# Performance work log

Hardware: AMD Instinct MI355X
Metric: run time of the kernel (lower is better)

## Reference

```python
import jax, jax.numpy as jnp
import numpy as np


def setup_inputs() -> dict:
    key = jax.random.key(0)
    ks = jax.random.split(key, 4)
    B, S, H = 1, 2048, 2048
    E, I = 32, 768
    scale_h = 1.0 / np.sqrt(H)
    scale_i = 1.0 / np.sqrt(I)
    return {
        "hidden_states": jax.random.normal(ks[0], (B, S, H), dtype=jnp.float32),
        "gate_w": jax.random.normal(ks[1], (E, H), dtype=jnp.float32) * scale_h,
        "gate_up_proj": jax.random.normal(ks[2], (E, H, 2 * I), dtype=jnp.float32) * scale_h,
        "down_proj": jax.random.normal(ks[3], (E, I, H), dtype=jnp.float32) * scale_i,
    }


TOP_K = 4


def reference(hidden_states, gate_w, gate_up_proj, down_proj):
    B, S, H = hidden_states.shape
    x = hidden_states.reshape(-1, H)                      # [T, H]
    T = x.shape[0]

    # Router: softmax -> top-k -> renormalize -> scatter back to dense [T, E]
    router_logits = x @ gate_w.T                          # [T, E]
    probs = jax.nn.softmax(router_logits.astype(jnp.float32), axis=-1)
    top_w, top_idx = jax.lax.top_k(probs, TOP_K)          # [T, K]
    top_w = top_w / jnp.sum(top_w, axis=-1, keepdims=True)
    top_w = top_w.astype(x.dtype)
    router_weights = jnp.zeros_like(router_logits).at[
        jnp.arange(T)[:, None], top_idx
    ].set(top_w)                                          # [T, E]

    # Experts (eval path): every expert processes every token, then weight & sum.
    gate_up = jnp.einsum("th,ehi->eti", x, gate_up_proj)  # [E, T, 2I]
    gate, up = jnp.split(gate_up, 2, axis=-1)
    h = up * jax.nn.silu(gate)                            # [E, T, I]
    expert_out = jnp.einsum("eti,eih->eth", h, down_proj)  # [E, T, H]
    out = jnp.einsum("eth,te->th", expert_out, router_weights)  # [T, H]

    return out.reshape(B, S, H), router_logits
```

## Files before the change

### kernel.cpp

```cpp
#include <hip/hip_runtime.h>
#include <hip/hip_bf16.h>

#define T_TOK 2048
#define H_DIM 2048
#define E_NUM 32
#define I_DIM 768
#define TOPK  4
#define S4    (T_TOK * TOPK)

typedef __attribute__((ext_vector_type(8))) short bf16x8;
typedef __attribute__((ext_vector_type(4))) float f32x4;

__device__ __forceinline__ unsigned pk2(float a, float b) {
    __hip_bfloat16 ha = __float2bfloat16(a);
    __hip_bfloat16 hb = __float2bfloat16(b);
    unsigned short ua = *(unsigned short*)&ha;
    unsigned short ub = *(unsigned short*)&hb;
    return (unsigned)ua | ((unsigned)ub << 16);
}

#define MFMA16(a, b, c) __builtin_amdgcn_mfma_f32_16x16x32_bf16(a, b, c, 0, 0, 0)

__global__ __launch_bounds__(256) void zero_kernel(uint4* __restrict__ p, int n16)
{
    int i = blockIdx.x * 256 + threadIdx.x;
    if (i < n16) p[i] = (uint4){0u, 0u, 0u, 0u};
}

__global__ __launch_bounds__(64) void router_kernel(
    const float* __restrict__ x, const float* __restrict__ gate_w,
    float* __restrict__ logits_out, int* __restrict__ cnt,
    int* __restrict__ tok_list, float* __restrict__ tok_w)
{
    const int t = blockIdx.x;
    const int lane = threadIdx.x;
    __shared__ float xs[H_DIM];
    const float4* __restrict__ xv = (const float4*)(x + (size_t)t * H_DIM);
    float4* xsv = (float4*)xs;
#pragma unroll
    for (int i = 0; i < H_DIM / 4 / 64; ++i) xsv[lane + i * 64] = xv[lane + i * 64];
    __syncthreads();

    const int e = lane & 31;
    const int half = lane >> 5;
    const float4* __restrict__ wv = (const float4*)(gate_w + (size_t)e * H_DIM) + half * (H_DIM / 8);
    const float4* __restrict__ xh = ((const float4*)xs) + half * (H_DIM / 8);
    float acc = 0.f;
#pragma unroll 4
    for (int i = 0; i < H_DIM / 8; ++i) {
        float4 w4 = wv[i], x4 = xh[i];
        acc += w4.x * x4.x + w4.y * x4.y + w4.z * x4.z + w4.w * x4.w;
    }
    acc += __shfl_xor(acc, 32, 64);
    if (lane < 32) logits_out[(size_t)t * E_NUM + e] = acc;

    float v = acc;
    float topv[TOPK]; int topi[TOPK];
#pragma unroll
    for (int r = 0; r < TOPK; ++r) {
        float bv = v; int bi = e;
#pragma unroll
        for (int off = 16; off >= 1; off >>= 1) {
            float ov = __shfl_xor(bv, off, 32);
            int   oi = __shfl_xor(bi, off, 32);
            if (ov > bv || (ov == bv && oi < bi)) { bv = ov; bi = oi; }
        }
        topv[r] = bv; topi[r] = bi;
        if (e == bi) v = -1e30f;
    }
    if (lane == 0) {
        float w[TOPK]; float s = 0.f;
#pragma unroll
        for (int r = 0; r < TOPK; ++r) { w[r] = expf(topv[r] - topv[0]); s += w[r]; }
        float inv = 1.f / s;
#pragma unroll
        for (int r = 0; r < TOPK; ++r) {
            int pos = atomicAdd(&cnt[topi[r]], 1);
            tok_list[topi[r] * T_TOK + pos] = t;
            tok_w  [topi[r] * T_TOK + pos] = w[r] * inv;
        }
    }
}

__global__ void scan_kernel(const int* __restrict__ cnt, int* __restrict__ slot_base)
{
    if (threadIdx.x == 0) {
        int s = 0;
        for (int e = 0; e < E_NUM; ++e) { slot_base[e] = s; s += cnt[e]; }
        slot_base[E_NUM] = s;
    }
}

__global__ __launch_bounds__(256) void gather_kernel(
    const float* __restrict__ x, const int* __restrict__ cnt,
    const int* __restrict__ slot_base, const int* __restrict__ tok_list,
    unsigned short* __restrict__ xg_t)
{
    const int e = blockIdx.x;
    const int count = cnt[e];
    const int m0 = blockIdx.y * 8;
    if (m0 >= count) return;
    const int s8   = threadIdx.x >> 5;
    const int kc31 = threadIdx.x & 31;
    const int m = m0 + s8;
    if (m >= count) return;
    const int tok  = tok_list[e * T_TOK + m];
    const int slot = slot_base[e] + m;
    const float* __restrict__ src = x + (size_t)tok * H_DIM;
#pragma unroll
    for (int kcq = 0; kcq < 8; ++kcq) {
        const int kc = kcq * 32 + kc31;
        float4 a = *(const float4*)(src + kc * 8);
        float4 b = *(const float4*)(src + kc * 8 + 4);
        uint4 o;
        o.x = pk2(a.x, a.y); o.y = pk2(a.z, a.w);
        o.z = pk2(b.x, b.y); o.w = pk2(b.z, b.w);
        *(uint4*)(xg_t + ((size_t)kc * S4 + slot) * 8) = o;
    }
}

#define GU_NC (H_DIM / 128)
__global__ __launch_bounds__(512, 4) void gateup_mfma(
    const unsigned short* __restrict__ xg_t, const float* __restrict__ gup_w,
    const int* __restrict__ cnt, const int* __restrict__ slot_base,
    const float* __restrict__ tok_w, unsigned short* __restrict__ h_t)
{
    const int e  = blockIdx.x;
    const int nt = blockIdx.y;
    const int mt = blockIdx.z;
    const int count = cnt[e];
    if (mt * 256 >= count) return;
    const int tid  = threadIdx.x;
    const int lane = tid & 63;
    const int w    = tid >> 6;
    const int base = slot_base[e];
    const int l16  = lane & 15, lg = lane >> 4;

    __shared__ unsigned short Bls[2][2][16 * 32 * 8];
    __shared__ float wls[256];

    if (tid < 256) {
        int m = mt * 256 + tid; if (m >= count) m = count - 1;
        wls[tid] = tok_w[e * T_TOK + m];
    }

    int m0 = mt * 256 + w * 32 + l16;      if (m0 >= count) m0 = count - 1;
    int m1 = mt * 256 + w * 32 + 16 + l16; if (m1 >= count) m1 = count - 1;
    const unsigned short* a0b = xg_t + (size_t)(base + m0) * 8;
    const unsigned short* a1b = xg_t + (size_t)(base + m1) * 8;

    const int bhalf = tid >> 8;
    const int sub   = (tid >> 7) & 1;
    const int t7    = tid & 127;
    const int kb    = (t7 >> 3) * 2;
    const int n4    = (t7 & 7) * 4;
    const int k8    = kb & 7;
    const int kbh   = kb >> 3;
    const float* __restrict__ bbase =
        gup_w + ((size_t)e * H_DIM + kb) * (2 * I_DIM) + (size_t)bhalf * I_DIM + nt * 32 + n4;

    float4 sv0[2], sv1[2];

#define GU_LOAD(C) do { _Pragma("unroll") for (int q2 = 0; q2 < 2; ++q2) { \
        const int q = sub + q2 * 2; \
        const float* s_ = bbase + (size_t)((C) * 128 + q * 32) * (2 * I_DIM); \
        sv0[q2] = *(const float4*)s_; \
        sv1[q2] = *(const float4*)(s_ + 2 * I_DIM); } } while (0)
#define GU_WRITE(BUF) do { _Pragma("unroll") for (int q2 = 0; q2 < 2; ++q2) { \
        const int q = sub + q2 * 2; \
        unsigned short* bw_ = &Bls[BUF][bhalf][((q * 4 + kbh) * 32) * 8]; \
        float p0[4] = {sv0[q2].x, sv0[q2].y, sv0[q2].z, sv0[q2].w}; \
        float p1[4] = {sv1[q2].x, sv1[q2].y, sv1[q2].z, sv1[q2].w}; \
        _Pragma("unroll") for (int j = 0; j < 4; ++j) \
            *(unsigned*)&bw_[(n4 + j) * 8 + k8] = pk2(p0[j], p1[j]); } } while (0)

    f32x4 accg[2][2], accu[2][2];
#pragma unroll
    for (int i = 0; i < 2; ++i)
#pragma unroll
        for (int f = 0; f < 2; ++f) { accg[i][f] = {0.f,0.f,0.f,0.f}; accu[i][f] = {0.f,0.f,0.f,0.f}; }

    GU_LOAD(0);
    GU_WRITE(0);

    for (int c = 0; c < GU_NC; ++c) {
        const int buf = c & 1;
        __syncthreads();
        if (c + 1 < GU_NC) GU_LOAD(c + 1);
#pragma unroll
        for (int s = 0; s < 4; ++s) {
            const size_t aoff = (size_t)(c * 16 + s * 4 + lg) * (S4 * 8);
            bf16x8 a0 = *(const bf16x8*)(a0b + aoff);
            bf16x8 a1 = *(const bf16x8*)(a1b + aoff);
            const unsigned short* bg_ = &Bls[buf][0][((s * 4 + lg) * 32 + l16) * 8];
            const unsigned short* bu_ = &Bls[buf][1][((s * 4 + lg) * 32 + l16) * 8];
            bf16x8 g0 = *(const bf16x8*)(bg_);
            bf16x8 g1 = *(const bf16x8*)(bg_ + 128);
            bf16x8 u0 = *(const bf16x8*)(bu_);
            bf16x8 u1 = *(const bf16x8*)(bu_ + 128);
            accg[0][0] = MFMA16(a0, g0, accg[0][0]);
            accg[0][1] = MFMA16(a0, g1, accg[0][1]);
            accu[0][0] = MFMA16(a0, u0, accu[0][0]);
            accu[0][1] = MFMA16(a0, u1, accu[0][1]);
            accg[1][0] = MFMA16(a1, g0, accg[1][0]);
            accg[1][1] = MFMA16(a1, g1, accg[1][1]);
            accu[1][0] = MFMA16(a1, u0, accu[1][0]);
            accu[1][1] = MFMA16(a1, u1, accu[1][1]);
        }
        if (c + 1 < GU_NC) GU_WRITE((c + 1) & 1);
    }
#undef GU_LOAD
#undef GU_WRITE

#pragma unroll
    for (int i = 0; i < 2; ++i) {
        const int mloc = w * 32 + i * 16 + lg * 4;
#pragma unroll
        for (int r = 0; r < 4; ++r) {
            const int mrow = mt * 256 + mloc + r;
            if (mrow < count) {
                const float wgt = wls[mloc + r];
                const size_t slot = (size_t)(base + mrow);
#pragma unroll
                for (int f = 0; f < 2; ++f) {
                    const int col = nt * 32 + f * 16 + l16;
                    float g = accg[i][f][r], u = accu[i][f][r];
                    float sv = g / (1.f + expf(-g));
                    __hip_bfloat16 hb = __float2bfloat16(wgt * u * sv);
                    h_t[((size_t)(col >> 3) * S4 + slot) * 8 + (col & 7)] = *(unsigned short*)&hb;
                }
            }
        }
    }
}

#define DN_NC (I_DIM / 128)
__global__ __launch_bounds__(512, 4) void down_mfma(
    const unsigned short* __restrict__ h_t, const float* __restrict__ down_w,
    const int* __restrict__ cnt, const int* __restrict__ slot_base,
    const int* __restrict__ tok_list, float* __restrict__ out)
{
    const int e  = blockIdx.x;
    const int nt = blockIdx.y;
    const int mt = blockIdx.z;
    const int count = cnt[e];
    if (mt * 256 >= count) return;
    const int tid  = threadIdx.x;
    const int lane = tid & 63;
    const int w    = tid >> 6;
    const int base = slot_base[e];
    const int l16  = lane & 15, lg = lane >> 4;

    __shared__ unsigned short Bls[2][16 * 64 * 8];
    __shared__ int toks[256];

    if (tid < 256) {
        int m = mt * 256 + tid; if (m >= count) m = count - 1;
        toks[tid] = tok_list[e * T_TOK + m];
    }

    int m0 = mt * 256 + w * 32 + l16;      if (m0 >= count) m0 = count - 1;
    int m1 = mt * 256 + w * 32 + 16 + l16; if (m1 >= count) m1 = count - 1;
    const unsigned short* a0b = h_t + (size_t)(base + m0) * 8;
    const unsigned short* a1b = h_t + (size_t)(base + m1) * 8;

    const int sub = tid >> 8;
    const int t8  = tid & 255;
    const int kb  = (t8 >> 4) * 2;
    const int n4  = (t8 & 15) * 4;
    const int k8  = kb & 7;
    const int kbh = kb >> 3;
    const float* __restrict__ bbase =
        down_w + ((size_t)e * I_DIM + kb) * H_DIM + nt * 64 + n4;

    float4 sv0[2], sv1[2];

#define DN_LOAD(C) do { _Pragma("unroll") for (int q2 = 0; q2 < 2; ++q2) { \
        const int q = sub + q2 * 2; \
        const float* s_ = bbase + (size_t)((C) * 128 + q * 32) * H_DIM; \
        sv0[q2] = *(const float4*)s_; \
        sv1[q2] = *(const float4*)(s_ + H_DIM); } } while (0)
#define DN_WRITE(BUF) do { _Pragma("unroll") for (int q2 = 0; q2 < 2; ++q2) { \
        const int q = sub + q2 * 2; \
        unsigned short* bw_ = &Bls[BUF][((q * 4 + kbh) * 64) * 8]; \
        float p0[4] = {sv0[q2].x, sv0[q2].y, sv0[q2].z, sv0[q2].w}; \
        float p1[4] = {sv1[q2].x, sv1[q2].y, sv1[q2].z, sv1[q2].w}; \
        _Pragma("unroll") for (int j = 0; j < 4; ++j) \
            *(unsigned*)&bw_[(n4 + j) * 8 + k8] = pk2(p0[j], p1[j]); } } while (0)

    f32x4 acc[2][4];
#pragma unroll
    for (int i = 0; i < 2; ++i)
#pragma unroll
        for (int f = 0; f < 4; ++f) acc[i][f] = {0.f,0.f,0.f,0.f};

    DN_LOAD(0);
    DN_WRITE(0);

    for (int c = 0; c < DN_NC; ++c) {
        const int buf = c & 1;
        __syncthreads();
        if (c + 1 < DN_NC) DN_LOAD(c + 1);
#pragma unroll
        for (int s = 0; s < 4; ++s) {
            const size_t aoff = (size_t)(c * 16 + s * 4 + lg) * (S4 * 8);
            bf16x8 a0 = *(const bf16x8*)(a0b + aoff);
            bf16x8 a1 = *(const bf16x8*)(a1b + aoff);
            const unsigned short* bf_ = &Bls[buf][((s * 4 + lg) * 64 + l16) * 8];
            bf16x8 b0 = *(const bf16x8*)(bf_);
            bf16x8 b1 = *(const bf16x8*)(bf_ + 128);
            bf16x8 b2 = *(const bf16x8*)(bf_ + 256);
            bf16x8 b3 = *(const bf16x8*)(bf_ + 384);
            acc[0][0] = MFMA16(a0, b0, acc[0][0]);
            acc[0][1] = MFMA16(a0, b1, acc[0][1]);
            acc[0][2] = MFMA16(a0, b2, acc[0][2]);
            acc[0][3] = MFMA16(a0, b3, acc[0][3]);
            acc[1][0] = MFMA16(a1, b0, acc[1][0]);
            acc[1][1] = MFMA16(a1, b1, acc[1][1]);
            acc[1][2] = MFMA16(a1, b2, acc[1][2]);
            acc[1][3] = MFMA16(a1, b3, acc[1][3]);
        }
        if (c + 1 < DN_NC) DN_WRITE((c + 1) & 1);
    }
#undef DN_LOAD
#undef DN_WRITE

#pragma unroll
    for (int i = 0; i < 2; ++i) {
        const int mloc = w * 32 + i * 16 + lg * 4;
#pragma unroll
        for (int r = 0; r < 4; ++r) {
            const int mrow = mt * 256 + mloc + r;
            if (mrow < count) {
                const int tok = toks[mloc + r];
#pragma unroll
                for (int f = 0; f < 4; ++f) {
                    const int col = nt * 64 + f * 16 + l16;
                    atomicAdd(&out[(size_t)tok * H_DIM + col], acc[i][f][r]);
                }
            }
        }
    }
}

extern "C" void kernel_launch(void* const* d_in, const int* in_sizes, int n_in,
                              void* d_out, int out_size, void* d_ws, size_t ws_size,
                              hipStream_t stream) {
    const float* x      = (const float*)d_in[0];
    const float* gate_w = (const float*)d_in[1];
    const float* gup_w  = (const float*)d_in[2];
    const float* down_w = (const float*)d_in[3];
    float* out    = (float*)d_out;

    char* wsp = (char*)d_ws;
    int*   cnt       = (int*)(wsp);
    int*   slot_base = (int*)(wsp + 256);
    int*   tok_list  = (int*)(wsp + 4096);
    float* tok_w     = (float*)(wsp + 4096 + (size_t)E_NUM * T_TOK * 4);
    unsigned short* xg_t = (unsigned short*)(wsp + (1u << 20));
    unsigned short* h_t  = (unsigned short*)(wsp + (1u << 20) + (size_t)S4 * H_DIM * 2);

    const int n16 = T_TOK * H_DIM / 4;
    zero_kernel<<<(n16 + 255) / 256, 256, 0, stream>>>((uint4*)out, n16);
    hipMemsetAsync(cnt, 0, 256, stream);

    router_kernel<<<T_TOK, 64, 0, stream>>>(x, gate_w, out + (size_t)T_TOK * H_DIM,
                                            cnt, tok_list, tok_w);
    scan_kernel<<<1, 64, 0, stream>>>(cnt, slot_base);
    gather_kernel<<<dim3(E_NUM, 256), 256, 0, stream>>>(x, cnt, slot_base, tok_list, xg_t);
    gateup_mfma<<<dim3(E_NUM, 24, 8), 512, 0, stream>>>(
        xg_t, gup_w, cnt, slot_base, tok_w, h_t);
    down_mfma<<<dim3(E_NUM, 32, 8), 512, 0, stream>>>(
        h_t, down_w, cnt, slot_base, tok_list, out);
}
```

Before: 467.6 us.

## Replace atomic scatter-add in down projection with slot buffer and combine kernel

The down-projection kernel now writes each routed row's output into a dense per-slot buffer instead of doing float atomicAdds into the output. A new combine kernel then sums the four expert rows for each token, using slot indices recorded by the router. This removes the output-zeroing kernel and the atomic contention, at the cost of a 64MB intermediate write and read plus one more kernel launch.

```diff
diff --git a/kernel.cpp b/kernel.cpp
--- a/kernel.cpp
+++ b/kernel.cpp
@@ -21,16 +21,11 @@
 
 #define MFMA16(a, b, c) __builtin_amdgcn_mfma_f32_16x16x32_bf16(a, b, c, 0, 0, 0)
 
-__global__ __launch_bounds__(256) void zero_kernel(uint4* __restrict__ p, int n16)
-{
-    int i = blockIdx.x * 256 + threadIdx.x;
-    if (i < n16) p[i] = (uint4){0u, 0u, 0u, 0u};
-}
-
 __global__ __launch_bounds__(64) void router_kernel(
     const float* __restrict__ x, const float* __restrict__ gate_w,
     float* __restrict__ logits_out, int* __restrict__ cnt,
-    int* __restrict__ tok_list, float* __restrict__ tok_w)
+    int* __restrict__ tok_list, float* __restrict__ tok_w,
+    int* __restrict__ tok_slots)
 {
     const int t = blockIdx.x;
     const int lane = threadIdx.x;
@@ -78,6 +73,7 @@
             int pos = atomicAdd(&cnt[topi[r]], 1);
             tok_list[topi[r] * T_TOK + pos] = t;
             tok_w  [topi[r] * T_TOK + pos] = w[r] * inv;
+            tok_slots[t * TOPK + r] = (topi[r] << 12) | pos;
         }
     }
 }
@@ -238,7 +234,7 @@
 __global__ __launch_bounds__(512, 4) void down_mfma(
     const unsigned short* __restrict__ h_t, const float* __restrict__ down_w,
     const int* __restrict__ cnt, const int* __restrict__ slot_base,
-    const int* __restrict__ tok_list, float* __restrict__ out)
+    float* __restrict__ ods)
 {
     const int e  = blockIdx.x;
     const int nt = blockIdx.y;
@@ -252,12 +248,6 @@
     const int l16  = lane & 15, lg = lane >> 4;
 
     __shared__ unsigned short Bls[2][16 * 64 * 8];
-    __shared__ int toks[256];
-
-    if (tid < 256) {
-        int m = mt * 256 + tid; if (m >= count) m = count - 1;
-        toks[tid] = tok_list[e * T_TOK + m];
-    }
 
     int m0 = mt * 256 + w * 32 + l16;      if (m0 >= count) m0 = count - 1;
     int m1 = mt * 256 + w * 32 + 16 + l16; if (m1 >= count) m1 = count - 1;
@@ -332,15 +322,39 @@
         for (int r = 0; r < 4; ++r) {
             const int mrow = mt * 256 + mloc + r;
             if (mrow < count) {
-                const int tok = toks[mloc + r];
-#pragma unroll
-                for (int f = 0; f < 4; ++f) {
-                    const int col = nt * 64 + f * 16 + l16;
-                    atomicAdd(&out[(size_t)tok * H_DIM + col], acc[i][f][r]);
-                }
+                float* orow = ods + (size_t)(base + mrow) * H_DIM + nt * 64;
+#pragma unroll
+                for (int f = 0; f < 4; ++f)
+                    orow[f * 16 + l16] = acc[i][f][r];
             }
         }
     }
+}
+
+__global__ __launch_bounds__(256) void combine_kernel(
+    const float* __restrict__ ods, const int* __restrict__ tok_slots,
+    const int* __restrict__ slot_base, float* __restrict__ out)
+{
+    const int t = blockIdx.x;
+    const int c0 = threadIdx.x * 8;
+    const float* rows[TOPK];
+#pragma unroll
+    for (int r = 0; r < TOPK; ++r) {
+        const int pk = tok_slots[t * TOPK + r];
+        const int e = pk >> 12, pos = pk & 4095;
+        rows[r] = ods + (size_t)(slot_base[e] + pos) * H_DIM + c0;
+    }
+    float4 a0 = {0.f,0.f,0.f,0.f}, a1 = {0.f,0.f,0.f,0.f};
+#pragma unroll
+    for (int r = 0; r < TOPK; ++r) {
+        float4 v0 = *(const float4*)(rows[r]);
+        float4 v1 = *(const float4*)(rows[r] + 4);
+        a0.x += v0.x; a0.y += v0.y; a0.z += v0.z; a0.w += v0.w;
+        a1.x += v1.x; a1.y += v1.y; a1.z += v1.z; a1.w += v1.w;
+    }
+    float* o = out + (size_t)t * H_DIM + c0;
+    *(float4*)o = a0;
+    *(float4*)(o + 4) = a1;
 }
 
 extern "C" void kernel_launch(void* const* d_in, const int* in_sizes, int n_in,
@@ -357,19 +371,20 @@
     int*   slot_base = (int*)(wsp + 256);
     int*   tok_list  = (int*)(wsp + 4096);
     float* tok_w     = (float*)(wsp + 4096 + (size_t)E_NUM * T_TOK * 4);
+    int*   tok_slots = (int*)(wsp + (768u << 10));
     unsigned short* xg_t = (unsigned short*)(wsp + (1u << 20));
     unsigned short* h_t  = (unsigned short*)(wsp + (1u << 20) + (size_t)S4 * H_DIM * 2);
-
-    const int n16 = T_TOK * H_DIM / 4;
-    zero_kernel<<<(n16 + 255) / 256, 256, 0, stream>>>((uint4*)out, n16);
+    float* ods = (float*)(wsp + (1u << 20) + (size_t)S4 * H_DIM * 2 + (size_t)S4 * I_DIM * 2);
+
     hipMemsetAsync(cnt, 0, 256, stream);
 
     router_kernel<<<T_TOK, 64, 0, stream>>>(x, gate_w, out + (size_t)T_TOK * H_DIM,
-                                            cnt, tok_list, tok_w);
+                                            cnt, tok_list, tok_w, tok_slots);
     scan_kernel<<<1, 64, 0, stream>>>(cnt, slot_base);
     gather_kernel<<<dim3(E_NUM, 256), 256, 0, stream>>>(x, cnt, slot_base, tok_list, xg_t);
     gateup_mfma<<<dim3(E_NUM, 24, 8), 512, 0, stream>>>(
         xg_t, gup_w, cnt, slot_base, tok_w, h_t);
     down_mfma<<<dim3(E_NUM, 32, 8), 512, 0, stream>>>(
-        h_t, down_w, cnt, slot_base, tok_list, out);
-}
+        h_t, down_w, cnt, slot_base, ods);
+    combine_kernel<<<T_TOK, 256, 0, stream>>>(ods, tok_slots, slot_base, out);
+}
```

Result: no change. 458.7 us (-1.9%).
